# Kernel optimization log

Hardware: AMD Instinct MI355X
Metric: run time of the kernel (lower is better)

## Reference

```python
import jax, jax.numpy as jnp
import numpy as np

B, S, H, NH, PF, L = 2, 2048, 1024, 16, 4096, 6
HD = H // NH
EPS = 1e-5


def setup_inputs() -> dict:
    key = jax.random.key(0)
    ks = jax.random.split(key, 12)
    s = lambda k, shp, fan: jax.random.normal(k, shp, jnp.float32) * (1.0 / np.sqrt(fan))
    return {
        "input_tensor": jax.random.normal(ks[0], (B, S, H), jnp.float32),
        "pos_emb": s(ks[1], (S, H), H),
        "Wq": s(ks[2], (L, H, H), H), "bq": jnp.zeros((L, H), jnp.float32),
        "Wk": s(ks[3], (L, H, H), H), "bk": jnp.zeros((L, H), jnp.float32),
        "Wv": s(ks[4], (L, H, H), H), "bv": jnp.zeros((L, H), jnp.float32),
        "Wo": s(ks[5], (L, H, H), H), "bo": jnp.zeros((L, H), jnp.float32),
        "ln_g": jnp.ones((L, H), jnp.float32), "ln_b": jnp.zeros((L, H), jnp.float32),
        "W1": s(ks[6], (L, H, PF), H), "b1": jnp.zeros((L, PF), jnp.float32),
        "W2": s(ks[7], (L, PF, H), PF), "b2": jnp.zeros((L, H), jnp.float32),
    }


def _layernorm(x, g, b):
    mu = jnp.mean(x, axis=-1, keepdims=True)
    var = jnp.mean(jnp.square(x - mu), axis=-1, keepdims=True)
    return (x - mu) * jax.lax.rsqrt(var + EPS) * g + b


def _encoder(input_tensor, pos_emb, params):
    # pos embed: same positions for every batch row
    src = input_tensor * jnp.sqrt(jnp.float32(H)) + pos_emb[None, :, :]

    def layer(src, p):
        Wq, bq, Wk, bk, Wv, bv, Wo, bo, g, b, W1, b1, W2, b2 = p
        q = (src @ Wq + bq).reshape(B, S, NH, HD)
        k = (src @ Wk + bk).reshape(B, S, NH, HD)
        v = (src @ Wv + bv).reshape(B, S, NH, HD)
        # scores [B, NH, S, S]
        energy = jnp.einsum("bqhd,bkhd->bhqk", q, k) / jnp.sqrt(jnp.float32(HD))
        attn = jax.nn.softmax(energy, axis=-1)
        ctx = jnp.einsum("bhqk,bkhd->bqhd", attn, v).reshape(B, S, H)
        attn_out = ctx @ Wo + bo
        src = _layernorm(src + attn_out, g, b)
        ffn = jax.nn.relu(src @ W1 + b1) @ W2 + b2
        src = _layernorm(src + ffn, g, b)  # same LayerNorm reused, as in source
        return src, None

    src, _ = jax.lax.scan(layer, src, params)
    return src


def reference(input_tensor, pos_emb, Wq, bq, Wk, bk, Wv, bv, Wo, bo, ln_g, ln_b, W1, b1, W2, b2):
    params = (Wq, bq, Wk, bk, Wv, bv, Wo, bo, ln_g, ln_b, W1, b1, W2, b2)
    return _encoder(input_tensor, pos_emb, params)
```

## Files before the change

kernel.cpp:

```cpp
#include <hip/hip_runtime.h>
#include <cstdint>

constexpr int Bc = 2, Sc = 2048, Hc = 1024, NHc = 16, HDc = 64, PFc = 4096, Lc = 6;
constexpr float EPSc = 1e-5f;
constexpr float QSC = 0.18033688011112042f;

using f32x4  = __attribute__((ext_vector_type(4))) float;
using bf16x8 = __attribute__((ext_vector_type(8))) __bf16;
using bf16x4 = __attribute__((ext_vector_type(4))) __bf16;
using u32x4  = __attribute__((ext_vector_type(4))) unsigned;

#if __has_builtin(__builtin_amdgcn_exp2f)
#define EXP2(x) __builtin_amdgcn_exp2f(x)
#else
#define EXP2(x) exp2f(x)
#endif

__device__ __forceinline__ f32x4 mfma16(bf16x8 a, bf16x8 b, f32x4 c) {
    return __builtin_amdgcn_mfma_f32_16x16x32_bf16(a, b, c, 0, 0, 0);
}

__device__ __forceinline__ void gload_lds16(const void* g, void* l) {
    __builtin_amdgcn_global_load_lds(
        (__attribute__((address_space(1))) void*)(uintptr_t)g,
        (__attribute__((address_space(3))) void*)(uint32_t)(uintptr_t)l,
        16, 0, 0);
}

struct HL { __bf16 h, l; };
__device__ __forceinline__ HL split2(float v) {
    HL r;
    r.h = (__bf16)v;
    r.l = (__bf16)(v - (float)r.h);
    return r;
}

__device__ __forceinline__ unsigned bfbits(__bf16 x) {
    return (unsigned)__builtin_bit_cast(unsigned short, x);
}
__device__ __forceinline__ unsigned packbf(float a, float b) {
    return bfbits((__bf16)a) | (bfbits((__bf16)b) << 16);
}

__device__ __forceinline__ int xcd_swz(int bid, int nwg) {
    return (bid & 7) * (nwg >> 3) + (bid >> 3);
}

__global__ __launch_bounds__(256) void wconv_kernel(
    const float* __restrict__ in, __bf16* __restrict__ out, int K, int N)
{
    __shared__ float tile[64][65];
    const int t = threadIdx.x;
    const size_t lstride = (size_t)K * N;
    const float* ip = in + (size_t)blockIdx.z * lstride;
    __bf16* op = out + (size_t)blockIdx.z * lstride;
    const int n0 = blockIdx.x * 64, k0 = blockIdx.y * 64;
    #pragma unroll
    for (int c = 0; c < 4; ++c) {
        int idx = c * 256 + t;
        int row = idx >> 4;
        int c4  = idx & 15;
        float4 v = *(const float4*)(ip + (size_t)(k0 + row) * N + n0 + c4 * 4);
        tile[row][c4 * 4 + 0] = v.x; tile[row][c4 * 4 + 1] = v.y;
        tile[row][c4 * 4 + 2] = v.z; tile[row][c4 * 4 + 3] = v.w;
    }
    __syncthreads();
    #pragma unroll
    for (int c = 0; c < 4; ++c) {
        int idx = c * 256 + t;
        int n  = idx >> 4;
        int k4 = idx & 15;
        bf16x4 hh = { (__bf16)tile[k4 * 4 + 0][n], (__bf16)tile[k4 * 4 + 1][n],
                      (__bf16)tile[k4 * 4 + 2][n], (__bf16)tile[k4 * 4 + 3][n] };
        *(bf16x4*)(op + (size_t)(n0 + n) * K + k0 + k4 * 4) = hh;
    }
}

__global__ __launch_bounds__(256) void wconv2_kernel(
    const float* __restrict__ in, __bf16* __restrict__ outh,
    __bf16* __restrict__ outl, int K, int N)
{
    __shared__ float tile[64][65];
    const int t = threadIdx.x;
    const int n0 = blockIdx.x * 64, k0 = blockIdx.y * 64;
    #pragma unroll
    for (int c = 0; c < 4; ++c) {
        int idx = c * 256 + t;
        int row = idx >> 4;
        int c4  = idx & 15;
        float4 v = *(const float4*)(in + (size_t)(k0 + row) * N + n0 + c4 * 4);
        tile[row][c4 * 4 + 0] = v.x; tile[row][c4 * 4 + 1] = v.y;
        tile[row][c4 * 4 + 2] = v.z; tile[row][c4 * 4 + 3] = v.w;
    }
    __syncthreads();
    #pragma unroll
    for (int c = 0; c < 4; ++c) {
        int idx = c * 256 + t;
        int n  = idx >> 4;
        int k4 = idx & 15;
        HL e0 = split2(tile[k4 * 4 + 0][n]);
        HL e1 = split2(tile[k4 * 4 + 1][n]);
        HL e2 = split2(tile[k4 * 4 + 2][n]);
        HL e3 = split2(tile[k4 * 4 + 3][n]);
        bf16x4 hh = { e0.h, e1.h, e2.h, e3.h };
        bf16x4 ll = { e0.l, e1.l, e2.l, e3.l };
        *(bf16x4*)(outh + (size_t)(n0 + n) * K + k0 + k4 * 4) = hh;
        *(bf16x4*)(outl + (size_t)(n0 + n) * K + k0 + k4 * 4) = ll;
    }
}

__global__ __launch_bounds__(256) void embed_kernel(
    const float* __restrict__ in, const float* __restrict__ pos,
    float* __restrict__ sf, __bf16* __restrict__ sh, __bf16* __restrict__ sl)
{
    const int n4 = (Bc * Sc * Hc) / 4;
    const int pmask = (Sc * Hc / 4) - 1;
    for (int i = blockIdx.x * 256 + threadIdx.x; i < n4; i += gridDim.x * 256) {
        float4 a = ((const float4*)in)[i];
        float4 p = ((const float4*)pos)[i & pmask];
        float4 r;
        r.x = a.x * 32.f + p.x; r.y = a.y * 32.f + p.y;
        r.z = a.z * 32.f + p.z; r.w = a.w * 32.f + p.w;
        ((float4*)sf)[i] = r;
        HL e0 = split2(r.x), e1 = split2(r.y), e2 = split2(r.z), e3 = split2(r.w);
        bf16x4 hh = { e0.h, e1.h, e2.h, e3.h };
        bf16x4 ll = { e0.l, e1.l, e2.l, e3.l };
        ((bf16x4*)sh)[i] = hh;
        ((bf16x4*)sl)[i] = ll;
    }
}

template<int BM, int OUTMODE, bool RELU>
__global__ __launch_bounds__(256) void gemm_bt_kernel(
    const __bf16* __restrict__ A, const __bf16* __restrict__ Wt,
    const float* __restrict__ bias, void* __restrict__ out,
    int M, int N, int K)
{
    constexpr int MI = BM / 32;
    __shared__ alignas(16) __bf16 Alds[2][BM * 64];
    __shared__ alignas(16) __bf16 Blds[2][128 * 64];

    const int tid = threadIdx.x, lane = tid & 63, wave = tid >> 6;
    const int lr = lane & 15, lg = lane >> 4;
    const int nbx = gridDim.x;
    const int swz = xcd_swz(blockIdx.y * nbx + blockIdx.x, nbx * gridDim.y);
    const int m0 = (swz / nbx) * BM, n0 = (swz % nbx) * 128;
    const int wm = (wave >> 1) * (BM / 2), wn = (wave & 1) * 64;

    f32x4 acc[MI][4] = {};

    auto stage = [&](int k0, int buf) {
        #pragma unroll
        for (int c = 0; c < BM / 32; ++c) {
            int li = c * 256 + tid;
            int row = li >> 3;
            int lcb = ((li & 7) << 4) ^ ((row & 7) << 4);
            gload_lds16(A + (size_t)(m0 + row) * K + k0 + (lcb >> 1),
                        (char*)Alds[buf] + (size_t)(c * 256 + wave * 64) * 16);
        }
        #pragma unroll
        for (int c = 0; c < 4; ++c) {
            int li = c * 256 + tid;
            int row = li >> 3;
            int lcb = ((li & 7) << 4) ^ ((row & 7) << 4);
            gload_lds16(Wt + (size_t)(n0 + row) * K + k0 + (lcb >> 1),
                        (char*)Blds[buf] + (size_t)(c * 256 + wave * 64) * 16);
        }
    };

    stage(0, 0);
    __syncthreads();
    int cur = 0;

    for (int k0 = 0; k0 < K; k0 += 64) {
        if (k0 + 64 < K) stage(k0 + 64, cur ^ 1);

        bf16x8 af[2][MI], bfr[2][4];
        #pragma unroll
        for (int ks = 0; ks < 2; ++ks) {
            #pragma unroll
            for (int i = 0; i < MI; ++i) {
                int ra = wm + i * 16 + lr;
                int pa = (ks * 64 + lg * 16) ^ ((ra & 7) << 4);
                af[ks][i] = *(const bf16x8*)((const char*)Alds[cur] + ra * 128 + pa);
            }
            #pragma unroll
            for (int i = 0; i < 4; ++i) {
                int rb = wn + i * 16 + lr;
                int pb = (ks * 64 + lg * 16) ^ ((rb & 7) << 4);
                bfr[ks][i] = *(const bf16x8*)((const char*)Blds[cur] + rb * 128 + pb);
            }
        }
        #pragma unroll
        for (int ks = 0; ks < 2; ++ks)
            #pragma unroll
            for (int mi = 0; mi < MI; ++mi)
                #pragma unroll
                for (int ni = 0; ni < 4; ++ni)
                    acc[mi][ni] = mfma16(af[ks][mi], bfr[ks][ni], acc[mi][ni]);

        __syncthreads();
        cur ^= 1;
    }

    #pragma unroll
    for (int ni = 0; ni < 4; ++ni) {
        int col = n0 + wn + ni * 16 + lr;
        float bv = bias[col];
        #pragma unroll
        for (int mi = 0; mi < MI; ++mi) {
            int rowb = m0 + wm + mi * 16 + lg * 4;
            #pragma unroll
            for (int r = 0; r < 4; ++r) {
                float v = acc[mi][ni][r] + bv;
                if (RELU) v = fmaxf(v, 0.f);
                size_t idx = (size_t)(rowb + r) * N + col;
                if constexpr (OUTMODE == 0) ((float*)out)[idx] = v;
                else                        ((__bf16*)out)[idx] = (__bf16)v;
            }
        }
    }
}

struct QKVBT {
    const __bf16 *wq, *wk, *wv;
    const float *bq, *bk, *bv;
    __bf16 *q, *k, *v;
};

__global__ __launch_bounds__(256) void qkv_bt_kernel(
    const __bf16* __restrict__ A, QKVBT a)
{
    constexpr int N = Hc, K = Hc;
    __shared__ alignas(16) __bf16 Alds[2][128 * 64];
    __shared__ alignas(16) __bf16 Blds[2][128 * 64];

    const int tid = threadIdx.x, lane = tid & 63, wave = tid >> 6;
    const int lr = lane & 15, lg = lane >> 4;
    const int nbx = gridDim.x;
    const int swz = xcd_swz(blockIdx.y * nbx + blockIdx.x, nbx * gridDim.y);
    const int gx = swz % nbx;
    const int widx = gx >> 3;
    const int n0 = (gx & 7) * 128;
    const int m0 = (swz / nbx) * 128;
    const int wm = (wave >> 1) * 64, wn = (wave & 1) * 64;

    const __bf16* Wt  = (widx == 0) ? a.wq : (widx == 1) ? a.wk : a.wv;
    const float* bias = (widx == 0) ? a.bq : (widx == 1) ? a.bk : a.bv;

    f32x4 acc[4][4] = {};

    auto stage = [&](int k0, int buf) {
        #pragma unroll
        for (int c = 0; c < 4; ++c) {
            int li = c * 256 + tid;
            int row = li >> 3;
            int lcb = ((li & 7) << 4) ^ ((row & 7) << 4);
            gload_lds16(A + (size_t)(m0 + row) * K + k0 + (lcb >> 1),
                        (char*)Alds[buf] + (size_t)(c * 256 + wave * 64) * 16);
            gload_lds16(Wt + (size_t)(n0 + row) * K + k0 + (lcb >> 1),
                        (char*)Blds[buf] + (size_t)(c * 256 + wave * 64) * 16);
        }
    };

    stage(0, 0);
    __syncthreads();
    int cur = 0;

    for (int k0 = 0; k0 < K; k0 += 64) {
        if (k0 + 64 < K) stage(k0 + 64, cur ^ 1);

        bf16x8 af[2][4], bfr[2][4];
        #pragma unroll
        for (int ks = 0; ks < 2; ++ks) {
            #pragma unroll
            for (int i = 0; i < 4; ++i) {
                int ra = wm + i * 16 + lr;
                int pa = (ks * 64 + lg * 16) ^ ((ra & 7) << 4);
                af[ks][i] = *(const bf16x8*)((const char*)Alds[cur] + ra * 128 + pa);
                int rb = wn + i * 16 + lr;
                int pb = (ks * 64 + lg * 16) ^ ((rb & 7) << 4);
                bfr[ks][i] = *(const bf16x8*)((const char*)Blds[cur] + rb * 128 + pb);
            }
        }
        #pragma unroll
        for (int ks = 0; ks < 2; ++ks)
            #pragma unroll
            for (int mi = 0; mi < 4; ++mi)
                #pragma unroll
                for (int ni = 0; ni < 4; ++ni)
                    acc[mi][ni] = mfma16(af[ks][mi], bfr[ks][ni], acc[mi][ni]);

        __syncthreads();
        cur ^= 1;
    }

    __bf16* outp = (widx == 0) ? a.q : (widx == 1) ? a.k : a.v;
    const float osc = (widx == 0) ? QSC : 1.f;
    #pragma unroll
    for (int ni = 0; ni < 4; ++ni) {
        int col = n0 + wn + ni * 16 + lr;
        float bv = bias[col];
        int hh = col >> 6, d = col & 63;
        #pragma unroll
        for (int mi = 0; mi < 4; ++mi) {
            int rowb = m0 + wm + mi * 16 + lg * 4;
            #pragma unroll
            for (int r = 0; r < 4; ++r) {
                int row = rowb + r;
                int bb = row >> 11, s = row & (Sc - 1);
                outp[((size_t)(bb * NHc + hh) * Sc + s) * HDc + d] =
                    (__bf16)((acc[mi][ni][r] + bv) * osc);
            }
        }
    }
}

struct QKV0S {
    const __bf16 *wqh, *wql, *wkh, *wkl, *wv;
    const float *bq, *bk, *bv;
    __bf16 *qh, *ql, *kh, *kl, *vv;
};

__global__ __launch_bounds__(256) void qkv0s_kernel(
    const __bf16* __restrict__ Ahi, const __bf16* __restrict__ Alo, QKV0S a)
{
    constexpr int N = Hc, K = Hc;
    __shared__ alignas(16) __bf16 AldsH[128 * 64];
    __shared__ alignas(16) __bf16 AldsL[128 * 64];
    __shared__ alignas(16) __bf16 BldsH[128 * 64];
    __shared__ alignas(16) __bf16 BldsL[128 * 64];

    const int tid = threadIdx.x, lane = tid & 63, wave = tid >> 6;
    const int lr = lane & 15, lg = lane >> 4;
    const int nbx = gridDim.x;
    const int swz = xcd_swz(blockIdx.y * nbx + blockIdx.x, nbx * gridDim.y);
    const int gx = swz % nbx;
    const int widx = gx >> 3;
    const int n0 = (gx & 7) * 128;
    const int m0 = (swz / nbx) * 128;
    const int wm = (wave >> 1) * 64, wn = (wave & 1) * 64;
    const bool SPLIT = (widx < 2);

    const __bf16* Bh = (widx == 0) ? a.wqh : (widx == 1) ? a.wkh : a.wv;
    const __bf16* Bl = (widx == 0) ? a.wql : a.wkl;
    const float* bias = (widx == 0) ? a.bq : (widx == 1) ? a.bk : a.bv;

    f32x4 acc[4][4] = {};

    for (int k0 = 0; k0 < K; k0 += 64) {
        #pragma unroll
        for (int c = 0; c < 4; ++c) {
            int li = c * 256 + tid;
            int row = li >> 3;
            int lcb = ((li & 7) << 4) ^ ((row & 7) << 4);
            size_t aoff = (size_t)(m0 + row) * K + k0 + (lcb >> 1);
            size_t boff = (size_t)(n0 + row) * K + k0 + (lcb >> 1);
            size_t loff = (size_t)(c * 256 + wave * 64) * 16;
            gload_lds16(Ahi + aoff, (char*)AldsH + loff);
            gload_lds16(Bh + boff, (char*)BldsH + loff);
            if (SPLIT) {
                gload_lds16(Alo + aoff, (char*)AldsL + loff);
                gload_lds16(Bl + boff, (char*)BldsL + loff);
            }
        }
        __syncthreads();

        bf16x8 ah[2][4], al[2][4], bh[2][4], bl[2][4];
        #pragma unroll
        for (int ks = 0; ks < 2; ++ks) {
            #pragma unroll
            for (int i = 0; i < 4; ++i) {
                int ra = wm + i * 16 + lr;
                int pa = (ks * 64 + lg * 16) ^ ((ra & 7) << 4);
                ah[ks][i] = *(const bf16x8*)((const char*)AldsH + ra * 128 + pa);
                int rb = wn + i * 16 + lr;
                int pb = (ks * 64 + lg * 16) ^ ((rb & 7) << 4);
                bh[ks][i] = *(const bf16x8*)((const char*)BldsH + rb * 128 + pb);
                if (SPLIT) {
                    al[ks][i] = *(const bf16x8*)((const char*)AldsL + ra * 128 + pa);
                    bl[ks][i] = *(const bf16x8*)((const char*)BldsL + rb * 128 + pb);
                }
            }
        }
        #pragma unroll
        for (int ks = 0; ks < 2; ++ks)
            #pragma unroll
            for (int mi = 0; mi < 4; ++mi)
                #pragma unroll
                for (int ni = 0; ni < 4; ++ni) {
                    acc[mi][ni] = mfma16(ah[ks][mi], bh[ks][ni], acc[mi][ni]);
                    if (SPLIT) {
                        acc[mi][ni] = mfma16(al[ks][mi], bh[ks][ni], acc[mi][ni]);
                        acc[mi][ni] = mfma16(ah[ks][mi], bl[ks][ni], acc[mi][ni]);
                    }
                }
        __syncthreads();
    }

    __bf16* outh = (widx == 0) ? a.qh : (widx == 1) ? a.kh : a.vv;
    __bf16* outl = (widx == 0) ? a.ql : a.kl;
    const float osc = (widx == 0) ? QSC : 1.f;
    #pragma unroll
    for (int ni = 0; ni < 4; ++ni) {
        int col = n0 + wn + ni * 16 + lr;
        float bv = bias[col];
        int hh = col >> 6, d = col & 63;
        #pragma unroll
        for (int mi = 0; mi < 4; ++mi) {
            int rowb = m0 + wm + mi * 16 + lg * 4;
            #pragma unroll
            for (int r = 0; r < 4; ++r) {
                int row = rowb + r;
                int bb = row >> 11, s = row & (Sc - 1);
                size_t idx = ((size_t)(bb * NHc + hh) * Sc + s) * HDc + d;
                float v = (acc[mi][ni][r] + bv) * osc;
                if (SPLIT) {
                    HL e = split2(v);
                    outh[idx] = e.h;
                    outl[idx] = e.l;
                } else {
                    outh[idx] = (__bf16)v;
                }
            }
        }
    }
}

template<int QKSPLIT, int NH2>
__global__ __launch_bounds__(256) void attn_kernel(
    const __bf16* __restrict__ Qh, const __bf16* __restrict__ Ql,
    const __bf16* __restrict__ Kh, const __bf16* __restrict__ Kl,
    const __bf16* __restrict__ V, __bf16* __restrict__ O)
{
    constexpr int KVB = 64 * NH2;
    __shared__ alignas(16) __bf16 Ksh[2][KVB * 64];
    __shared__ alignas(16) __bf16 Klo[QKSPLIT ? 2 : 1][QKSPLIT ? 64 * 64 : 8];
    __shared__ alignas(16) __bf16 VT[2][NH2][64 * 64];

    const int tid = threadIdx.x;
    const int lane = tid & 63, wave = tid >> 6;
    const int lr = lane & 15, lg = lane >> 4;
    const int h = blockIdx.y, b = blockIdx.z;
    const int q0 = blockIdx.x * 128 + wave * 32;

    const size_t headoff = ((size_t)b * NHc + h) * Sc * HDc;
    const __bf16* Qb  = Qh + headoff;
    const __bf16* Kb  = Kh + headoff;
    const __bf16* Klb = QKSPLIT ? (Kl + headoff) : nullptr;
    const __bf16* Vb  = V + headoff;

    const size_t qrowA = (size_t)(q0 + lr) * HDc;
    const size_t qrowB = qrowA + 16 * HDc;
    bf16x8 qfA0 = *(const bf16x8*)(Qb + qrowA + lg * 8);
    bf16x8 qfA1 = *(const bf16x8*)(Qb + qrowA + 32 + lg * 8);
    bf16x8 qfB0 = *(const bf16x8*)(Qb + qrowB + lg * 8);
    bf16x8 qfB1 = *(const bf16x8*)(Qb + qrowB + 32 + lg * 8);
    bf16x8 qlA0, qlA1, qlB0, qlB1;
    if constexpr (QKSPLIT) {
        const __bf16* Qlb = Ql + headoff;
        qlA0 = *(const bf16x8*)(Qlb + qrowA + lg * 8);
        qlA1 = *(const bf16x8*)(Qlb + qrowA + 32 + lg * 8);
        qlB0 = *(const bf16x8*)(Qlb + qrowB + lg * 8);
        qlB1 = *(const bf16x8*)(Qlb + qrowB + 32 + lg * 8);
    }

    const int kp = tid & 31, dblk = tid >> 5;
    const int sp = (kp & 0x11) | ((kp & 0x06) << 1) | ((kp & 0x08) >> 2);

    auto stageK = [&](int kt, int buf) {
        #pragma unroll
        for (int c = 0; c < 2 * NH2; ++c) {
            int li  = c * 256 + tid;
            int row = li >> 3;
            int lcb = ((li & 7) << 4) ^ ((row & 7) << 4);
            size_t goff = (size_t)(kt * KVB + row) * HDc + (lcb >> 1);
            size_t loff = (size_t)(c * 256 + wave * 64) * 16;
            gload_lds16(Kb + goff, (char*)Ksh[buf] + loff);
            if constexpr (QKSPLIT)
                gload_lds16(Klb + goff, (char*)Klo[buf] + loff);
        }
    };
    auto loadV = [&](int kt, int half, bf16x8& va, bf16x8& vb2) {
        const __bf16* vs = Vb + (size_t)(kt * KVB + half * 64 + 2 * kp) * HDc + dblk * 8;
        va  = *(const bf16x8*)vs;
        vb2 = *(const bf16x8*)(vs + HDc);
    };
    auto writeVT = [&](int buf, int half, bf16x8 va, bf16x8 vb2) {
        #pragma unroll
        for (int j = 0; j < 8; ++j) {
            int d = dblk * 8 + j;
            unsigned u = bfbits(va[j]) | (bfbits(vb2[j]) << 16);
            int byte = d * 128 + ((sp * 4) ^ ((d & 7) << 4));
            *(unsigned*)((char*)VT[buf][half] + byte) = u;
        }
    };

    f32x4 oA[4] = {}, oB[4] = {};
    float mA = -1e30f, mB = -1e30f, lsA = 0.f, lsB = 0.f;

    stageK(0, 0);
    {
        bf16x8 va, vb2;
        #pragma unroll
        for (int hf = 0; hf < NH2; ++hf) {
            loadV(0, hf, va, vb2);
            writeVT(0, hf, va, vb2);
        }
    }
    __syncthreads();

    const int NT = Sc / KVB;
    int cur = 0;
    for (int kt = 0; kt < NT; ++kt) {
        const int nb = cur ^ 1;
        const bool pf = (kt + 1 < NT);
        bf16x8 va[NH2], vb2[NH2];
        if (pf) {
            stageK(kt + 1, nb);
            #pragma unroll
            for (int hf = 0; hf < NH2; ++hf) loadV(kt + 1, hf, va[hf], vb2[hf]);
        }

        const char* Kc  = (const char*)Ksh[cur];
        const char* Klc = (const char*)Klo[QKSPLIT ? cur : 0];

        #pragma unroll
        for (int half = 0; half < NH2; ++half) {
            f32x4 sA[4], sB[4];
            __builtin_amdgcn_s_setprio(1);
            #pragma unroll
            for (int kg = 0; kg < 4; ++kg) {
                int ra = half * 64 + kg * 16 + lr;
                int pa0 = (lg * 16) ^ ((ra & 7) << 4);
                int pa1 = (64 + lg * 16) ^ ((ra & 7) << 4);
                bf16x8 kf0 = *(const bf16x8*)(Kc + ra * 128 + pa0);
                bf16x8 kf1 = *(const bf16x8*)(Kc + ra * 128 + pa1);
                f32x4 tA = {}, tB = {};
                tA = mfma16(kf0, qfA0, tA);
                tA = mfma16(kf1, qfA1, tA);
                tB = mfma16(kf0, qfB0, tB);
                tB = mfma16(kf1, qfB1, tB);
                if constexpr (QKSPLIT) {
                    bf16x8 kg0 = *(const bf16x8*)(Klc + ra * 128 + pa0);
                    bf16x8 kg1 = *(const bf16x8*)(Klc + ra * 128 + pa1);
                    tA = mfma16(kg0, qfA0, tA);
                    tA = mfma16(kg1, qfA1, tA);
                    tA = mfma16(kf0, qlA0, tA);
                    tA = mfma16(kf1, qlA1, tA);
                    tB = mfma16(kg0, qfB0, tB);
                    tB = mfma16(kg1, qfB1, tB);
                    tB = mfma16(kf0, qlB0, tB);
                    tB = mfma16(kf1, qlB1, tB);
                }
                sA[kg] = tA;
                sB[kg] = tB;
            }
            __builtin_amdgcn_s_setprio(0);

            float mtA = -1e30f, mtB = -1e30f;
            #pragma unroll
            for (int kg = 0; kg < 4; ++kg)
                #pragma unroll
                for (int r = 0; r < 4; ++r) {
                    mtA = fmaxf(mtA, sA[kg][r]);
                    mtB = fmaxf(mtB, sB[kg][r]);
                }
            mtA = fmaxf(mtA, __shfl_xor(mtA, 16));
            mtA = fmaxf(mtA, __shfl_xor(mtA, 32));
            mtB = fmaxf(mtB, __shfl_xor(mtB, 16));
            mtB = fmaxf(mtB, __shfl_xor(mtB, 32));
            if (!__all(mtA <= mA + 8.f)) {
                float mnew = fmaxf(mA, mtA);
                float fac = EXP2(mA - mnew);
                mA = mnew;
                lsA *= fac;
                #pragma unroll
                for (int r = 0; r < 4; ++r) {
                    float fr = __shfl(fac, (lg << 4) | (lg * 4 + r));
                    #pragma unroll
                    for (int nd = 0; nd < 4; ++nd) oA[nd][r] *= fr;
                }
            }
            if (!__all(mtB <= mB + 8.f)) {
                float mnew = fmaxf(mB, mtB);
                float fac = EXP2(mB - mnew);
                mB = mnew;
                lsB *= fac;
                #pragma unroll
                for (int r = 0; r < 4; ++r) {
                    float fr = __shfl(fac, (lg << 4) | (lg * 4 + r));
                    #pragma unroll
                    for (int nd = 0; nd < 4; ++nd) oB[nd][r] *= fr;
                }
            }
            float psA = 0.f, psB = 0.f;
            #pragma unroll
            for (int kg = 0; kg < 4; ++kg)
                #pragma unroll
                for (int r = 0; r < 4; ++r) {
                    float pA = EXP2(sA[kg][r] - mA);
                    float pB = EXP2(sB[kg][r] - mB);
                    psA += pA;
                    psB += pB;
                    sA[kg][r] = pA;
                    sB[kg][r] = pB;
                }
            psA += __shfl_xor(psA, 16);
            psA += __shfl_xor(psA, 32);
            psB += __shfl_xor(psB, 16);
            psB += __shfl_xor(psB, 32);
            lsA += psA;
            lsB += psB;

            #pragma unroll
            for (int kh2 = 0; kh2 < 2; ++kh2) {
                u32x4 pkA, pkB;
                pkA[0] = packbf(sA[2 * kh2][0],     sA[2 * kh2][1]);
                pkA[1] = packbf(sA[2 * kh2][2],     sA[2 * kh2][3]);
                pkA[2] = packbf(sA[2 * kh2 + 1][0], sA[2 * kh2 + 1][1]);
                pkA[3] = packbf(sA[2 * kh2 + 1][2], sA[2 * kh2 + 1][3]);
                pkB[0] = packbf(sB[2 * kh2][0],     sB[2 * kh2][1]);
                pkB[1] = packbf(sB[2 * kh2][2],     sB[2 * kh2][3]);
                pkB[2] = packbf(sB[2 * kh2 + 1][0], sB[2 * kh2 + 1][1]);
                pkB[3] = packbf(sB[2 * kh2 + 1][2], sB[2 * kh2 + 1][3]);
                bf16x8 pafA = __builtin_bit_cast(bf16x8, pkA);
                bf16x8 pafB = __builtin_bit_cast(bf16x8, pkB);
                __builtin_amdgcn_s_setprio(1);
                #pragma unroll
                for (int nd = 0; nd < 4; ++nd) {
                    int d = nd * 16 + lr;
                    int byte = d * 128 + ((64 * kh2 + 16 * lg) ^ ((d & 7) << 4));
                    bf16x8 vbf = *(const bf16x8*)((const char*)VT[cur][half] + byte);
                    oA[nd] = mfma16(pafA, vbf, oA[nd]);
                    oB[nd] = mfma16(pafB, vbf, oB[nd]);
                }
                __builtin_amdgcn_s_setprio(0);
            }
        }

        if (pf) {
            #pragma unroll
            for (int hf = 0; hf < NH2; ++hf) writeVT(nb, hf, va[hf], vb2[hf]);
        }
        __syncthreads();
        cur = nb;
    }

    #pragma unroll
    for (int r = 0; r < 4; ++r) {
        float lvA = __shfl(lsA, (lg << 4) | (lg * 4 + r));
        float lvB = __shfl(lsB, (lg << 4) | (lg * 4 + r));
        float invA = 1.f / lvA;
        float invB = 1.f / lvB;
        size_t orowA = ((size_t)b * Sc + q0 + lg * 4 + r) * Hc + h * HDc;
        size_t orowB = orowA + (size_t)16 * Hc;
        #pragma unroll
        for (int nd = 0; nd < 4; ++nd) {
            O[orowA + nd * 16 + lr] = (__bf16)(oA[nd][r] * invA);
            O[orowB + nd * 16 + lr] = (__bf16)(oB[nd][r] * invB);
        }
    }
}

__global__ __launch_bounds__(256) void ln_kernel(
    const float* __restrict__ xr, const __bf16* __restrict__ y,
    const float* __restrict__ g, const float* __restrict__ beta,
    float* __restrict__ of, __bf16* __restrict__ oh)
{
    __shared__ float red[2][4];
    const int row = blockIdx.x, t = threadIdx.x;
    const int lane = t & 63, wave = t >> 6;
    const int idx = row * 256 + t;
    float4 a = ((const float4*)xr)[idx];
    bf16x4 cb = ((const bf16x4*)y)[idx];
    float4 v;
    v.x = a.x + (float)cb[0]; v.y = a.y + (float)cb[1];
    v.z = a.z + (float)cb[2]; v.w = a.w + (float)cb[3];
    float s1 = v.x + v.y + v.z + v.w;
    float s2 = v.x * v.x + v.y * v.y + v.z * v.z + v.w * v.w;
    #pragma unroll
    for (int off = 1; off < 64; off <<= 1) {
        s1 += __shfl_xor(s1, off);
        s2 += __shfl_xor(s2, off);
    }
    if (lane == 0) { red[0][wave] = s1; red[1][wave] = s2; }
    __syncthreads();
    s1 = red[0][0] + red[0][1] + red[0][2] + red[0][3];
    s2 = red[1][0] + red[1][1] + red[1][2] + red[1][3];
    const float mu   = s1 * (1.f / Hc);
    const float var  = s2 * (1.f / Hc) - mu * mu;
    const float rstd = rsqrtf(var + EPSc);
    float4 gg = ((const float4*)g)[t];
    float4 bb = ((const float4*)beta)[t];
    float4 r;
    r.x = (v.x - mu) * rstd * gg.x + bb.x;
    r.y = (v.y - mu) * rstd * gg.y + bb.y;
    r.z = (v.z - mu) * rstd * gg.z + bb.z;
    r.w = (v.w - mu) * rstd * gg.w + bb.w;
    ((float4*)of)[idx] = r;
    bf16x4 hh = { (__bf16)r.x, (__bf16)r.y, (__bf16)r.z, (__bf16)r.w };
    ((bf16x4*)oh)[idx] = hh;
}

extern "C" void kernel_launch(void* const* d_in, const int* in_sizes, int n_in,
                              void* d_out, int out_size, void* d_ws, size_t ws_size,
                              hipStream_t stream)
{
    const float* inp = (const float*)d_in[0];
    const float* pos = (const float*)d_in[1];
    const float* Wq  = (const float*)d_in[2];
    const float* bq  = (const float*)d_in[3];
    const float* Wk  = (const float*)d_in[4];
    const float* bk  = (const float*)d_in[5];
    const float* Wv  = (const float*)d_in[6];
    const float* bv  = (const float*)d_in[7];
    const float* Wo  = (const float*)d_in[8];
    const float* bo  = (const float*)d_in[9];
    const float* lng = (const float*)d_in[10];
    const float* lnb = (const float*)d_in[11];
    const float* W1  = (const float*)d_in[12];
    const float* b1  = (const float*)d_in[13];
    const float* W2  = (const float*)d_in[14];
    const float* b2  = (const float*)d_in[15];

    char* ws = (char*)d_ws;
    const size_t MB = 1u << 20;
    float*  src_f = (float*)(ws);
    __bf16* src_h = (__bf16*)(ws + 16 * MB);
    __bf16* src_l = (__bf16*)(ws + 24 * MB);
    __bf16* qh    = (__bf16*)(ws + 32 * MB);
    __bf16* kh    = (__bf16*)(ws + 40 * MB);
    __bf16* vv    = (__bf16*)(ws + 48 * MB);
    __bf16* ctx   = (__bf16*)(ws + 56 * MB);
    __bf16* ql    = (__bf16*)(ws + 64 * MB);
    __bf16* kl    = (__bf16*)(ws + 72 * MB);
    __bf16* tmpb  = (__bf16*)(ws + 80 * MB);
    __bf16* wq0h  = (__bf16*)(ws + 80 * MB);
    __bf16* wq0l  = (__bf16*)(ws + 82 * MB);
    __bf16* wk0h  = (__bf16*)(ws + 84 * MB);
    __bf16* wk0l  = (__bf16*)(ws + 86 * MB);
    __bf16* h1    = (__bf16*)(ws + 32 * MB);
    __bf16* wqT   = (__bf16*)(ws + 96 * MB);
    __bf16* wkT   = (__bf16*)(ws + 108 * MB);
    __bf16* wvT   = (__bf16*)(ws + 120 * MB);
    __bf16* woT   = (__bf16*)(ws + 132 * MB);
    __bf16* w1T   = (__bf16*)(ws + 144 * MB);
    __bf16* w2T   = (__bf16*)(ws + 192 * MB);

    const int M = Bc * Sc;

    wconv_kernel<<<dim3(16, 16, 6), 256, 0, stream>>>(Wq, wqT, Hc, Hc);
    wconv_kernel<<<dim3(16, 16, 6), 256, 0, stream>>>(Wk, wkT, Hc, Hc);
    wconv_kernel<<<dim3(16, 16, 6), 256, 0, stream>>>(Wv, wvT, Hc, Hc);
    wconv_kernel<<<dim3(16, 16, 6), 256, 0, stream>>>(Wo, woT, Hc, Hc);
    wconv_kernel<<<dim3(64, 16, 6), 256, 0, stream>>>(W1, w1T, Hc, PFc);
    wconv_kernel<<<dim3(16, 64, 6), 256, 0, stream>>>(W2, w2T, PFc, Hc);
    wconv2_kernel<<<dim3(16, 16), 256, 0, stream>>>(Wq, wq0h, wq0l, Hc, Hc);
    wconv2_kernel<<<dim3(16, 16), 256, 0, stream>>>(Wk, wk0h, wk0l, Hc, Hc);

    embed_kernel<<<2048, 256, 0, stream>>>(inp, pos, src_f, src_h, src_l);

    for (int l = 0; l < Lc; ++l) {
        const size_t wHH = (size_t)l * Hc * Hc;
        const size_t wH  = (size_t)l * Hc;
        if (l == 0) {
            QKV0S qa = { wq0h, wq0l, wk0h, wk0l, wvT, bq, bk, bv,
                         qh, ql, kh, kl, vv };
            qkv0s_kernel<<<dim3(24, 32), 256, 0, stream>>>(src_h, src_l, qa);
            attn_kernel<1, 1><<<dim3(16, 16, 2), 256, 0, stream>>>(qh, ql, kh, kl, vv, ctx);
        } else {
            QKVBT qa = { wqT + wHH, wkT + wHH, wvT + wHH, bq + wH, bk + wH, bv + wH,
                         qh, kh, vv };
            qkv_bt_kernel<<<dim3(24, 32), 256, 0, stream>>>(src_h, qa);
            attn_kernel<0, 2><<<dim3(16, 16, 2), 256, 0, stream>>>(qh, nullptr, kh, nullptr, vv, ctx);
        }
        gemm_bt_kernel<64, 1, false><<<dim3(8, 64), 256, 0, stream>>>(
            ctx, woT + wHH, bo + wH, tmpb, M, Hc, Hc);
        ln_kernel<<<M, 256, 0, stream>>>(src_f, tmpb, lng + wH, lnb + wH, src_f, src_h);
        gemm_bt_kernel<128, 1, true><<<dim3(32, 32), 256, 0, stream>>>(
            src_h, w1T + (size_t)l * Hc * PFc, b1 + (size_t)l * PFc, h1, M, PFc, Hc);
        gemm_bt_kernel<64, 1, false><<<dim3(8, 64), 256, 0, stream>>>(
            h1, w2T + (size_t)l * PFc * Hc, b2 + wH, tmpb, M, Hc, PFc);
        float* dst = (l == Lc - 1) ? (float*)d_out : src_f;
        ln_kernel<<<M, 256, 0, stream>>>(src_f, tmpb, lng + wH, lnb + wH, dst, src_h);
    }
}
```

Measured before the change: 1.586 ms.

## Prefetch two K-tiles ahead with vmcnt waits and remap attention grid

The GEMM and QKV kernels now issue loads two K-tiles ahead. Each iteration waits on vmcnt counters and raw s_barrier instead of __syncthreads, and the MFMA block is wrapped in raised wave priority, so global-to-LDS loads overlap compute more deeply. The attention launch becomes a flat 1D grid with head and batch in the low bits, so blocks sharing a query tile position but different heads are scheduled together. The hand-tuned waitcnt values must match the exact number of loads per stage; the wait_vmcnt template only emits an instruction for 0, 6 and 8, so any other tile size would silently skip the wait.

Result: faster. 1.508 ms (-4.9%).

```diff
diff --git a/kernel.cpp b/kernel.cpp
--- a/kernel.cpp
+++ b/kernel.cpp
@@ -25,6 +25,16 @@
         (__attribute__((address_space(1))) void*)(uintptr_t)g,
         (__attribute__((address_space(3))) void*)(uint32_t)(uintptr_t)l,
         16, 0, 0);
+}
+
+template<int N> __device__ __forceinline__ void wait_vmcnt() {
+    if constexpr (N == 0)      asm volatile("s_waitcnt vmcnt(0)" ::: "memory");
+    else if constexpr (N == 6) asm volatile("s_waitcnt vmcnt(6)" ::: "memory");
+    else if constexpr (N == 8) asm volatile("s_waitcnt vmcnt(8)" ::: "memory");
+}
+__device__ __forceinline__ void wait_lgkm0() {
+    asm volatile("s_waitcnt lgkmcnt(0)" ::: "memory");
+    __builtin_amdgcn_sched_barrier(0);
 }
 
 struct HL { __bf16 h, l; };
@@ -137,6 +147,7 @@
     int M, int N, int K)
 {
     constexpr int MI = BM / 32;
+    constexpr int LPT = BM / 32 + 4;
     __shared__ alignas(16) __bf16 Alds[2][BM * 64];
     __shared__ alignas(16) __bf16 Blds[2][128 * 64];
 
@@ -169,11 +180,13 @@
     };
 
     stage(0, 0);
-    __syncthreads();
-    int cur = 0;
+    if (K > 64) stage(64, 1);
 
     for (int k0 = 0; k0 < K; k0 += 64) {
-        if (k0 + 64 < K) stage(k0 + 64, cur ^ 1);
+        const int cur = (k0 >> 6) & 1;
+        if (k0 + 64 < K) wait_vmcnt<LPT>();
+        else             wait_vmcnt<0>();
+        __builtin_amdgcn_s_barrier();
 
         bf16x8 af[2][MI], bfr[2][4];
         #pragma unroll
@@ -191,6 +204,11 @@
                 bfr[ks][i] = *(const bf16x8*)((const char*)Blds[cur] + rb * 128 + pb);
             }
         }
+        wait_lgkm0();
+        __builtin_amdgcn_s_barrier();
+        if (k0 + 128 < K) stage(k0 + 128, cur);
+
+        __builtin_amdgcn_s_setprio(1);
         #pragma unroll
         for (int ks = 0; ks < 2; ++ks)
             #pragma unroll
@@ -198,9 +216,7 @@
                 #pragma unroll
                 for (int ni = 0; ni < 4; ++ni)
                     acc[mi][ni] = mfma16(af[ks][mi], bfr[ks][ni], acc[mi][ni]);
-
-        __syncthreads();
-        cur ^= 1;
+        __builtin_amdgcn_s_setprio(0);
     }
 
     #pragma unroll
@@ -232,6 +248,7 @@
     const __bf16* __restrict__ A, QKVBT a)
 {
     constexpr int N = Hc, K = Hc;
+    constexpr int LPT = 8;
     __shared__ alignas(16) __bf16 Alds[2][128 * 64];
     __shared__ alignas(16) __bf16 Blds[2][128 * 64];
 
@@ -264,11 +281,13 @@
     };
 
     stage(0, 0);
-    __syncthreads();
-    int cur = 0;
+    stage(64, 1);
 
     for (int k0 = 0; k0 < K; k0 += 64) {
-        if (k0 + 64 < K) stage(k0 + 64, cur ^ 1);
+        const int cur = (k0 >> 6) & 1;
+        if (k0 + 64 < K) wait_vmcnt<LPT>();
+        else             wait_vmcnt<0>();
+        __builtin_amdgcn_s_barrier();
 
         bf16x8 af[2][4], bfr[2][4];
         #pragma unroll
@@ -283,6 +302,11 @@
                 bfr[ks][i] = *(const bf16x8*)((const char*)Blds[cur] + rb * 128 + pb);
             }
         }
+        wait_lgkm0();
+        __builtin_amdgcn_s_barrier();
+        if (k0 + 128 < K) stage(k0 + 128, cur);
+
+        __builtin_amdgcn_s_setprio(1);
         #pragma unroll
         for (int ks = 0; ks < 2; ++ks)
             #pragma unroll
@@ -290,9 +314,7 @@
                 #pragma unroll
                 for (int ni = 0; ni < 4; ++ni)
                     acc[mi][ni] = mfma16(af[ks][mi], bfr[ks][ni], acc[mi][ni]);
-
-        __syncthreads();
-        cur ^= 1;
+        __builtin_amdgcn_s_setprio(0);
     }
 
     __bf16* outp = (widx == 0) ? a.q : (widx == 1) ? a.k : a.v;
@@ -441,8 +463,10 @@
     const int tid = threadIdx.x;
     const int lane = tid & 63, wave = tid >> 6;
     const int lr = lane & 15, lg = lane >> 4;
-    const int h = blockIdx.y, b = blockIdx.z;
-    const int q0 = blockIdx.x * 128 + wave * 32;
+    const int flat = blockIdx.x;
+    const int hb = flat & 31;
+    const int h = hb & 15, b = hb >> 4;
+    const int q0 = (flat >> 5) * 128 + wave * 32;
 
     const size_t headoff = ((size_t)b * NHc + h) * Sc * HDc;
     const __bf16* Qb  = Qh + headoff;
@@ -768,12 +792,12 @@
             QKV0S qa = { wq0h, wq0l, wk0h, wk0l, wvT, bq, bk, bv,
                          qh, ql, kh, kl, vv };
             qkv0s_kernel<<<dim3(24, 32), 256, 0, stream>>>(src_h, src_l, qa);
-            attn_kernel<1, 1><<<dim3(16, 16, 2), 256, 0, stream>>>(qh, ql, kh, kl, vv, ctx);
+            attn_kernel<1, 1><<<512, 256, 0, stream>>>(qh, ql, kh, kl, vv, ctx);
         } else {
             QKVBT qa = { wqT + wHH, wkT + wHH, wvT + wHH, bq + wH, bk + wH, bv + wH,
                          qh, kh, vv };
             qkv_bt_kernel<<<dim3(24, 32), 256, 0, stream>>>(src_h, qa);
-            attn_kernel<0, 2><<<dim3(16, 16, 2), 256, 0, stream>>>(qh, nullptr, kh, nullptr, vv, ctx);
+            attn_kernel<0, 2><<<512, 256, 0, stream>>>(qh, nullptr, kh, nullptr, vv, ctx);
         }
         gemm_bt_kernel<64, 1, false><<<dim3(8, 64), 256, 0, stream>>>(
             ctx, woT + wHH, bo + wH, tmpb, M, Hc, Hc);
```
